# Kernel tuning notes

Measured on AMD Instinct MI355X. Metric: run time of the kernel, lower is better.

## Reference

```python
import jax, jax.numpy as jnp
import numpy as np

N = 50000
E = 640000
D_IN = 128
D_HID = 128
D_S = 64


def setup_inputs() -> dict:
    key = jax.random.key(0)
    ks = jax.random.split(key, 8)
    x = jax.random.normal(ks[0], (N, D_IN), dtype=jnp.float32)
    edge_index = jax.random.randint(ks[1], (2, E), 0, N, dtype=jnp.int64)
    # SAGEConv params: lin_l (applied to aggregated neighbors, has bias), lin_r (root)
    def glorot(k, fan_in, fan_out):
        lim = (6.0 / (fan_in + fan_out)) ** 0.5
        return jax.random.uniform(k, (fan_in, fan_out), jnp.float32, -lim, lim)
    return {
        "x": x,
        "edge_index": edge_index,
        "W_l1": glorot(ks[2], D_IN, D_HID),
        "b_l1": jnp.zeros((D_HID,), jnp.float32),
        "W_r1": glorot(ks[3], D_IN, D_HID),
        "W_l2": glorot(ks[4], D_HID, D_HID),
        "b_l2": jnp.zeros((D_HID,), jnp.float32),
        "W_r2": glorot(ks[5], D_HID, D_HID),
        "W_s": glorot(ks[6], D_HID, D_S),
    }


def _sage_conv(x, src, dst, W_l, b_l, W_r):
    # mean aggregation of source-node features into target nodes
    agg = jax.ops.segment_sum(x[src], dst, num_segments=N)  # [N, d]
    cnt = jax.ops.segment_sum(jnp.ones((src.shape[0],), x.dtype), dst, num_segments=N)
    mean = agg / jnp.maximum(cnt, 1.0)[:, None]
    return mean @ W_l + b_l + x @ W_r


def reference(x, edge_index, W_l1, b_l1, W_r1, W_l2, b_l2, W_r2, W_s):
    src, dst = edge_index[0], edge_index[1]
    h = _sage_conv(x, src, dst, W_l1, b_l1, W_r1)
    h = jax.nn.relu(h)
    h = _sage_conv(h, src, dst, W_l2, b_l2, W_r2)
    out_s = h @ W_s
    return (out_s, h)
```

## Files before the change

### kernel.cpp

```cpp
#include <hip/hip_runtime.h>

#define N_NODES 50000
#define E_EDGES 640000
#define D 128
#define DS 64
#define NTILES 3125
#define BUCKET 64
#define CPAD 16
#define NPART 8
#define PSIZE 6250

typedef __bf16 bf16x8 __attribute__((ext_vector_type(8)));
typedef float f32x4 __attribute__((ext_vector_type(4)));

static __device__ __forceinline__ ushort f2bf(float f) {
    uint u = __float_as_uint(f);
    uint r = u + 0x7fffu + ((u >> 16) & 1u);
    return (ushort)(r >> 16);
}


__global__ void prep_kernel(const float* __restrict__ x,
                            const float* __restrict__ Wl1, const float* __restrict__ Wr1,
                            const float* __restrict__ Wl2, const float* __restrict__ Wr2,
                            const float* __restrict__ Ws,
                            int* __restrict__ cursor, ushort* __restrict__ xb,
                            ushort* __restrict__ WT1f, ushort* __restrict__ WT2f,
                            ushort* __restrict__ WsTf) {
    int tid = blockIdx.x * blockDim.x + threadIdx.x;
    int stride = gridDim.x * blockDim.x;
    for (int i = tid; i < N_NODES * CPAD; i += stride) cursor[i] = 0;
    if (tid < 32768) {
        int n = tid >> 8, k = tid & 255;
        float v = (k < 128) ? Wl1[k * 128 + n] : Wr1[(k - 128) * 128 + n];
        int F = (n >> 4) * 8 + (k >> 5);
        int l = (n & 15) | (((k >> 3) & 3) << 4);
        WT1f[(F * 64 + l) * 8 + (k & 7)] = f2bf(v);
    } else if (tid < 65536) {
        int j = tid - 32768;
        int n = j >> 8, k = j & 255;
        float v = (k < 128) ? Wl2[k * 128 + n] : Wr2[(k - 128) * 128 + n];
        int F = (n >> 4) * 8 + (k >> 5);
        int l = (n & 15) | (((k >> 3) & 3) << 4);
        WT2f[(F * 64 + l) * 8 + (k & 7)] = f2bf(v);
    } else if (tid < 73728) {
        int j = tid - 65536;
        int m = j >> 7, k = j & 127;
        int F = (m >> 4) * 4 + (k >> 5);
        int l = (m & 15) | (((k >> 3) & 3) << 4);
        WsTf[(F * 64 + l) * 8 + (k & 7)] = f2bf(Ws[k * 64 + m]);
    }
    const int n4 = N_NODES * D / 4;
    for (int i = tid; i < n4; i += stride) {
        float4 v = ((const float4*)x)[i];
        ushort4 o;
        o.x = f2bf(v.x); o.y = f2bf(v.y); o.z = f2bf(v.z); o.w = f2bf(v.w);
        ((ushort4*)xb)[i] = o;
    }
}


__global__ void fill_part(const int* __restrict__ src, const int* __restrict__ dst,
                          int* __restrict__ cursor, ushort* __restrict__ esrc, int e) {
    int g = blockIdx.x & (NPART - 1);
    int bchunk = blockIdx.x >> 3;
    int lo = g * PSIZE, hi = lo + PSIZE;
    int nb = gridDim.x >> 3;
    int i = bchunk * blockDim.x + threadIdx.x;
    int stride = nb * blockDim.x;
    for (; i < e; i += stride) {
        int d = dst[i];
        if (d >= lo && d < hi) {
            int pos = atomicAdd(&cursor[d * CPAD], 1);
            if (pos < BUCKET) esrc[d * BUCKET + pos] = (ushort)src[i];
        }
    }
}


__global__ void aggregate_mean_bf16(const ushort* __restrict__ feat, const int* __restrict__ cursor,
                                    const ushort* __restrict__ esrc, ushort* __restrict__ mean, int n) {
    int wid = threadIdx.x >> 6;
    int lane = threadIdx.x & 63;
    int d = blockIdx.x * 4 + wid;
    if (d >= n) return;
    int cnt = cursor[d * CPAD]; if (cnt > BUCKET) cnt = BUCKET;
    int beg = d * BUCKET;
    int g = lane >> 4;
    int gl = lane & 15;

    float acc[8] = {0.f, 0.f, 0.f, 0.f, 0.f, 0.f, 0.f, 0.f};
    for (int i = 0; i < cnt; i += 16) {
        uint4 v[4];
#pragma unroll
        for (int j = 0; j < 4; ++j) {
            int idx = i + g + j * 4;
            v[j] = make_uint4(0u, 0u, 0u, 0u);
            if (idx < cnt) {
                int e = esrc[beg + idx];
                v[j] = ((const uint4*)(feat + (size_t)e * D))[gl];
            }
        }
#pragma unroll
        for (int j = 0; j < 4; ++j) {
            acc[0] += __uint_as_float(v[j].x << 16);
            acc[1] += __uint_as_float(v[j].x & 0xffff0000u);
            acc[2] += __uint_as_float(v[j].y << 16);
            acc[3] += __uint_as_float(v[j].y & 0xffff0000u);
            acc[4] += __uint_as_float(v[j].z << 16);
            acc[5] += __uint_as_float(v[j].z & 0xffff0000u);
            acc[6] += __uint_as_float(v[j].w << 16);
            acc[7] += __uint_as_float(v[j].w & 0xffff0000u);
        }
    }
#pragma unroll
    for (int m = 16; m <= 32; m <<= 1) {
#pragma unroll
        for (int j = 0; j < 8; ++j) acc[j] += __shfl_xor(acc[j], m);
    }
    if (g == 0) {
        float inv = (cnt > 0) ? 1.0f / (float)cnt : 0.0f;
        uint4 o;
        o.x = (uint)f2bf(acc[0] * inv) | ((uint)f2bf(acc[1] * inv) << 16);
        o.y = (uint)f2bf(acc[2] * inv) | ((uint)f2bf(acc[3] * inv) << 16);
        o.z = (uint)f2bf(acc[4] * inv) | ((uint)f2bf(acc[5] * inv) << 16);
        o.w = (uint)f2bf(acc[6] * inv) | ((uint)f2bf(acc[7] * inv) << 16);
        ((uint4*)(mean + (size_t)d * D))[gl] = o;
    }
}


template <bool RELU, bool WF32, bool WBF16, bool OUTS>
__global__ __launch_bounds__(512) void sage_mfma(
    const ushort* __restrict__ A1, const ushort* __restrict__ A2,
    const ushort* __restrict__ WTf, const float* __restrict__ bias,
    float* __restrict__ Hf, ushort* __restrict__ Hb,
    const ushort* __restrict__ WsTf, float* __restrict__ OutS)
{
    __shared__ __attribute__((aligned(16))) char smem[OUTS ? 81920 : 65536];
    int w = threadIdx.x >> 6, lane = threadIdx.x & 63;

#pragma unroll
    for (int it = 0; it < 8; ++it) {
        int off = w * 8192 + it * 1024;
        __builtin_amdgcn_global_load_lds(
            (const __attribute__((address_space(1))) void*)((const char*)WTf + off + lane * 16),
            (__attribute__((address_space(3))) void*)(smem + off), 16, 0, 0);
    }
    if (OUTS) {
#pragma unroll
        for (int it = 0; it < 2; ++it) {
            int off = w * 2048 + it * 1024;
            __builtin_amdgcn_global_load_lds(
                (const __attribute__((address_space(1))) void*)((const char*)WsTf + off + lane * 16),
                (__attribute__((address_space(3))) void*)(smem + 65536 + off), 16, 0, 0);
        }
    }

    int rl = lane & 15;
    int kg = lane >> 4;
    int tile = blockIdx.x * 8 + w;

    bf16x8 a[8];
    if (tile < NTILES) {
        const ushort* r1 = A1 + (size_t)(tile * 16 + rl) * 128 + kg * 8;
        const ushort* r2 = A2 + (size_t)(tile * 16 + rl) * 128 + kg * 8;
#pragma unroll
        for (int s = 0; s < 4; ++s) a[s] = *reinterpret_cast<const bf16x8*>(r1 + s * 32);
#pragma unroll
        for (int s = 0; s < 4; ++s) a[4 + s] = *reinterpret_cast<const bf16x8*>(r2 + s * 32);
    }
    __syncthreads();
    if (tile >= NTILES) return;

    f32x4 acc[8];
#pragma unroll
    for (int f = 0; f < 8; ++f)
        acc[f] = *reinterpret_cast<const f32x4*>(bias + f * 16 + kg * 4);

#pragma unroll
    for (int s = 0; s < 8; ++s) {
#pragma unroll
        for (int f = 0; f < 8; ++f) {
            bf16x8 b = *reinterpret_cast<const bf16x8*>(smem + ((f * 8 + s) * 64 + lane) * 16);
            acc[f] = __builtin_amdgcn_mfma_f32_16x16x32_bf16(b, a[s], acc[f], 0, 0, 0);
        }
    }

    int node = tile * 16 + rl;
#pragma unroll
    for (int f = 0; f < 8; ++f) {
        f32x4 v = acc[f];
        if (RELU) {
            v[0] = fmaxf(v[0], 0.f); v[1] = fmaxf(v[1], 0.f);
            v[2] = fmaxf(v[2], 0.f); v[3] = fmaxf(v[3], 0.f);
        }
        acc[f] = v;
        size_t o = (size_t)node * 128 + f * 16 + kg * 4;
        if (WF32)
            *reinterpret_cast<f32x4*>(Hf + o) = v;
        if (WBF16) {
            ushort4 ob;
            ob.x = f2bf(v[0]); ob.y = f2bf(v[1]); ob.z = f2bf(v[2]); ob.w = f2bf(v[3]);
            *reinterpret_cast<ushort4*>(Hb + o) = ob;
        }
    }

    if (OUTS) {
        uint abx[8], aby[8];
#pragma unroll
        for (int f = 0; f < 8; ++f) {
            abx[f] = (uint)f2bf(acc[f][0]) | ((uint)f2bf(acc[f][1]) << 16);
            aby[f] = (uint)f2bf(acc[f][2]) | ((uint)f2bf(acc[f][3]) << 16);
        }
        int sbase = rl + ((lane & 16) << 1);
        bool top = lane >= 32;
        f32x4 accO[4];
#pragma unroll
        for (int fo = 0; fo < 4; ++fo) accO[fo] = (f32x4){0.f, 0.f, 0.f, 0.f};

#pragma unroll
        for (int s = 0; s < 4; ++s) {
            uint lx = abx[s * 2], ly = aby[s * 2];
            uint hx = abx[s * 2 + 1], hy = aby[s * 2 + 1];
            uint l0 = (uint)__shfl((int)lx, sbase);
            uint h0 = (uint)__shfl((int)hx, sbase);
            uint l1 = (uint)__shfl((int)ly, sbase);
            uint h1 = (uint)__shfl((int)hy, sbase);
            uint l2 = (uint)__shfl((int)lx, sbase + 16);
            uint h2_ = (uint)__shfl((int)hx, sbase + 16);
            uint l3 = (uint)__shfl((int)ly, sbase + 16);
            uint h3 = (uint)__shfl((int)hy, sbase + 16);
            uint q0 = top ? h0 : l0;
            uint q1 = top ? h1 : l1;
            uint q2 = top ? h2_ : l2;
            uint q3 = top ? h3 : l3;
            union { uint4 u; bf16x8 b; } cvt;
            cvt.u = make_uint4(q0, q1, q2, q3);
#pragma unroll
            for (int fo = 0; fo < 4; ++fo) {
                bf16x8 wsA = *reinterpret_cast<const bf16x8*>(
                    smem + 65536 + ((fo * 4 + s) * 64 + lane) * 16);
                accO[fo] = __builtin_amdgcn_mfma_f32_16x16x32_bf16(wsA, cvt.b, accO[fo], 0, 0, 0);
            }
        }
#pragma unroll
        for (int fo = 0; fo < 4; ++fo)
            *reinterpret_cast<f32x4*>(OutS + (size_t)node * DS + fo * 16 + kg * 4) = accO[fo];
    }
}

extern "C" void kernel_launch(void* const* d_in, const int* in_sizes, int n_in,
                              void* d_out, int out_size, void* d_ws, size_t ws_size,
                              hipStream_t stream) {
    const float* x   = (const float*)d_in[0];
    const int*   ei  = (const int*)d_in[1];
    const float* Wl1 = (const float*)d_in[2];
    const float* bl1 = (const float*)d_in[3];
    const float* Wr1 = (const float*)d_in[4];
    const float* Wl2 = (const float*)d_in[5];
    const float* bl2 = (const float*)d_in[6];
    const float* Wr2 = (const float*)d_in[7];
    const float* Ws  = (const float*)d_in[8];

    const int* src = ei;
    const int* dst = ei + E_EDGES;

    char* wsb = (char*)d_ws;
    size_t off = 0;
    auto alloc = [&](size_t bytes) -> void* {
        void* p = wsb + off;
        off = (off + bytes + 255) & ~(size_t)255;
        return p;
    };
    int*    cursor = (int*)alloc(4 * (size_t)N_NODES * CPAD);
    ushort* esrc   = (ushort*)alloc(2 * (size_t)N_NODES * BUCKET);
    ushort* xb     = (ushort*)alloc(2 * (size_t)N_NODES * D);
    ushort* meanb  = (ushort*)alloc(2 * (size_t)N_NODES * D);
    ushort* h1b    = (ushort*)alloc(2 * (size_t)N_NODES * D);
    ushort* WT1f   = (ushort*)alloc(2 * 128 * 256);
    ushort* WT2f   = (ushort*)alloc(2 * 128 * 256);
    ushort* WsTf   = (ushort*)alloc(2 * 64 * 128);

    float* out_s = (float*)d_out;
    float* h2    = (float*)d_out + (size_t)N_NODES * DS;

    prep_kernel<<<2048, 256, 0, stream>>>(x, Wl1, Wr1, Wl2, Wr2, Ws,
                                          cursor, xb, WT1f, WT2f, WsTf);

    fill_part<<<1024, 256, 0, stream>>>(src, dst, cursor, esrc, E_EDGES);

    const int GB = (NTILES + 7) / 8;

    aggregate_mean_bf16<<<(N_NODES + 3) / 4, 256, 0, stream>>>(xb, cursor, esrc, meanb, N_NODES);
    sage_mfma<true, false, true, false><<<GB, 512, 0, stream>>>(
        meanb, xb, WT1f, bl1, nullptr, h1b, nullptr, nullptr);

    aggregate_mean_bf16<<<(N_NODES + 3) / 4, 256, 0, stream>>>(h1b, cursor, esrc, meanb, N_NODES);
    sage_mfma<false, true, false, true><<<GB, 512, 0, stream>>>(
        meanb, h1b, WT2f, bl2, h2, nullptr, WsTf, out_s);
}
```

Baseline: 124.7 us.

## Overlap edge bucketing with bf16 conversion in one combined launch

```diff
diff --git a/kernel.cpp b/kernel.cpp
--- a/kernel.cpp
+++ b/kernel.cpp
@@ -9,9 +9,12 @@
 #define CPAD 16
 #define NPART 8
 #define PSIZE 6250
+#define FILL_BLOCKS 1024
+#define PREP_BLOCKS 1024
 
 typedef __bf16 bf16x8 __attribute__((ext_vector_type(8)));
 typedef float f32x4 __attribute__((ext_vector_type(4)));
+typedef float f32x4v __attribute__((ext_vector_type(4)));
 
 static __device__ __forceinline__ ushort f2bf(float f) {
     uint u = __float_as_uint(f);
@@ -20,59 +23,67 @@
 }
 
 
-__global__ void prep_kernel(const float* __restrict__ x,
-                            const float* __restrict__ Wl1, const float* __restrict__ Wr1,
-                            const float* __restrict__ Wl2, const float* __restrict__ Wr2,
-                            const float* __restrict__ Ws,
-                            int* __restrict__ cursor, ushort* __restrict__ xb,
-                            ushort* __restrict__ WT1f, ushort* __restrict__ WT2f,
-                            ushort* __restrict__ WsTf) {
-    int tid = blockIdx.x * blockDim.x + threadIdx.x;
+__global__ void zero_cursor(int* __restrict__ p, int n) {
+    int i = blockIdx.x * blockDim.x + threadIdx.x;
     int stride = gridDim.x * blockDim.x;
-    for (int i = tid; i < N_NODES * CPAD; i += stride) cursor[i] = 0;
-    if (tid < 32768) {
-        int n = tid >> 8, k = tid & 255;
-        float v = (k < 128) ? Wl1[k * 128 + n] : Wr1[(k - 128) * 128 + n];
-        int F = (n >> 4) * 8 + (k >> 5);
-        int l = (n & 15) | (((k >> 3) & 3) << 4);
-        WT1f[(F * 64 + l) * 8 + (k & 7)] = f2bf(v);
-    } else if (tid < 65536) {
-        int j = tid - 32768;
-        int n = j >> 8, k = j & 255;
-        float v = (k < 128) ? Wl2[k * 128 + n] : Wr2[(k - 128) * 128 + n];
-        int F = (n >> 4) * 8 + (k >> 5);
-        int l = (n & 15) | (((k >> 3) & 3) << 4);
-        WT2f[(F * 64 + l) * 8 + (k & 7)] = f2bf(v);
-    } else if (tid < 73728) {
-        int j = tid - 65536;
-        int m = j >> 7, k = j & 127;
-        int F = (m >> 4) * 4 + (k >> 5);
-        int l = (m & 15) | (((k >> 3) & 3) << 4);
-        WsTf[(F * 64 + l) * 8 + (k & 7)] = f2bf(Ws[k * 64 + m]);
-    }
-    const int n4 = N_NODES * D / 4;
-    for (int i = tid; i < n4; i += stride) {
-        float4 v = ((const float4*)x)[i];
-        ushort4 o;
-        o.x = f2bf(v.x); o.y = f2bf(v.y); o.z = f2bf(v.z); o.w = f2bf(v.w);
-        ((ushort4*)xb)[i] = o;
-    }
-}
-
-
-__global__ void fill_part(const int* __restrict__ src, const int* __restrict__ dst,
-                          int* __restrict__ cursor, ushort* __restrict__ esrc, int e) {
-    int g = blockIdx.x & (NPART - 1);
-    int bchunk = blockIdx.x >> 3;
-    int lo = g * PSIZE, hi = lo + PSIZE;
-    int nb = gridDim.x >> 3;
-    int i = bchunk * blockDim.x + threadIdx.x;
-    int stride = nb * blockDim.x;
-    for (; i < e; i += stride) {
-        int d = dst[i];
-        if (d >= lo && d < hi) {
-            int pos = atomicAdd(&cursor[d * CPAD], 1);
-            if (pos < BUCKET) esrc[d * BUCKET + pos] = (ushort)src[i];
+    for (; i < n; i += stride) p[i] = 0;
+}
+
+
+__global__ void prep_fill(const int* __restrict__ src, const int* __restrict__ dst,
+                          int* __restrict__ cursor, ushort* __restrict__ esrc,
+                          const float* __restrict__ x,
+                          const float* __restrict__ Wl1, const float* __restrict__ Wr1,
+                          const float* __restrict__ Wl2, const float* __restrict__ Wr2,
+                          const float* __restrict__ Ws,
+                          ushort* __restrict__ xb,
+                          ushort* __restrict__ WT1f, ushort* __restrict__ WT2f,
+                          ushort* __restrict__ WsTf) {
+    if (blockIdx.x < FILL_BLOCKS) {
+        int g = blockIdx.x & (NPART - 1);
+        int bchunk = blockIdx.x >> 3;
+        int lo = g * PSIZE, hi = lo + PSIZE;
+        const int nb = FILL_BLOCKS >> 3;
+        int i = bchunk * blockDim.x + threadIdx.x;
+        const int stride = nb * blockDim.x;
+        for (; i < E_EDGES; i += stride) {
+            int d = __builtin_nontemporal_load(dst + i);
+            if (d >= lo && d < hi) {
+                int s = __builtin_nontemporal_load(src + i);
+                int pos = atomicAdd(&cursor[d * CPAD], 1);
+                if (pos < BUCKET) esrc[d * BUCKET + pos] = (ushort)s;
+            }
+        }
+    } else {
+        int bid = blockIdx.x - FILL_BLOCKS;
+        int tid = bid * blockDim.x + threadIdx.x;
+        if (tid < 32768) {
+            int n = tid >> 8, k = tid & 255;
+            float v = (k < 128) ? Wl1[k * 128 + n] : Wr1[(k - 128) * 128 + n];
+            int F = (n >> 4) * 8 + (k >> 5);
+            int l = (n & 15) | (((k >> 3) & 3) << 4);
+            WT1f[(F * 64 + l) * 8 + (k & 7)] = f2bf(v);
+        } else if (tid < 65536) {
+            int j = tid - 32768;
+            int n = j >> 8, k = j & 255;
+            float v = (k < 128) ? Wl2[k * 128 + n] : Wr2[(k - 128) * 128 + n];
+            int F = (n >> 4) * 8 + (k >> 5);
+            int l = (n & 15) | (((k >> 3) & 3) << 4);
+            WT2f[(F * 64 + l) * 8 + (k & 7)] = f2bf(v);
+        } else if (tid < 73728) {
+            int j = tid - 65536;
+            int m = j >> 7, k = j & 127;
+            int F = (m >> 4) * 4 + (k >> 5);
+            int l = (m & 15) | (((k >> 3) & 3) << 4);
+            WsTf[(F * 64 + l) * 8 + (k & 7)] = f2bf(Ws[k * 64 + m]);
+        }
+        const int n4 = N_NODES * D / 4;
+        const int pstride = PREP_BLOCKS * blockDim.x;
+        for (int i = tid; i < n4; i += pstride) {
+            f32x4v v = __builtin_nontemporal_load((const f32x4v*)x + i);
+            ushort4 o;
+            o.x = f2bf(v[0]); o.y = f2bf(v[1]); o.z = f2bf(v[2]); o.w = f2bf(v[3]);
+            ((ushort4*)xb)[i] = o;
         }
     }
 }
@@ -285,10 +296,9 @@
     float* out_s = (float*)d_out;
     float* h2    = (float*)d_out + (size_t)N_NODES * DS;
 
-    prep_kernel<<<2048, 256, 0, stream>>>(x, Wl1, Wr1, Wl2, Wr2, Ws,
-                                          cursor, xb, WT1f, WT2f, WsTf);
-
-    fill_part<<<1024, 256, 0, stream>>>(src, dst, cursor, esrc, E_EDGES);
+    zero_cursor<<<1024, 256, 0, stream>>>(cursor, N_NODES * CPAD);
+    prep_fill<<<FILL_BLOCKS + PREP_BLOCKS, 256, 0, stream>>>(
+        src, dst, cursor, esrc, x, Wl1, Wr1, Wl2, Wr2, Ws, xb, WT1f, WT2f, WsTf);
 
     const int GB = (NTILES + 7) / 8;
 
```

Measured after the change: 140.8 us. 1.13x slower.

## Pre-bin edges by destination partition before scattering into per-node buckets

Applied to the files above, without the earlier changes.

```diff
diff --git a/kernel.cpp b/kernel.cpp
--- a/kernel.cpp
+++ b/kernel.cpp
@@ -9,6 +9,7 @@
 #define CPAD 16
 #define NPART 8
 #define PSIZE 6250
+#define BCAP  98304
 
 typedef __bf16 bf16x8 __attribute__((ext_vector_type(8)));
 typedef float f32x4 __attribute__((ext_vector_type(4)));
@@ -24,12 +25,14 @@
                             const float* __restrict__ Wl1, const float* __restrict__ Wr1,
                             const float* __restrict__ Wl2, const float* __restrict__ Wr2,
                             const float* __restrict__ Ws,
-                            int* __restrict__ cursor, ushort* __restrict__ xb,
+                            int* __restrict__ cursor, int* __restrict__ bincnt,
+                            ushort* __restrict__ xb,
                             ushort* __restrict__ WT1f, ushort* __restrict__ WT2f,
                             ushort* __restrict__ WsTf) {
     int tid = blockIdx.x * blockDim.x + threadIdx.x;
     int stride = gridDim.x * blockDim.x;
     for (int i = tid; i < N_NODES * CPAD; i += stride) cursor[i] = 0;
+    if (tid < NPART * 16) bincnt[tid] = 0;
     if (tid < 32768) {
         int n = tid >> 8, k = tid & 255;
         float v = (k < 128) ? Wl1[k * 128 + n] : Wr1[(k - 128) * 128 + n];
@@ -60,20 +63,49 @@
 }
 
 
-__global__ void fill_part(const int* __restrict__ src, const int* __restrict__ dst,
-                          int* __restrict__ cursor, ushort* __restrict__ esrc, int e) {
+__global__ void bin_pass(const int* __restrict__ src, const int* __restrict__ dst,
+                         int* __restrict__ bincnt, uint* __restrict__ binned, int e) {
+    int lane = threadIdx.x & 63;
+    int i = blockIdx.x * blockDim.x + threadIdx.x;
+    int stride = gridDim.x * blockDim.x;
+    for (; i < e; i += stride) {
+        int d = dst[i];
+        int s = src[i];
+        int myp = d / PSIZE;
+        uint entry = ((uint)d << 16) | (uint)s;
+#pragma unroll
+        for (int p = 0; p < NPART; ++p) {
+            unsigned long long mask = __ballot(myp == p);
+            if (mask) {
+                int leader = __ffsll((long long)mask) - 1;
+                int cnt = __popcll(mask);
+                int base = 0;
+                if (lane == leader) base = atomicAdd(&bincnt[p * 16], cnt);
+                base = __shfl(base, leader);
+                int rank = __popcll(mask & ((1ull << lane) - 1ull));
+                int slot = base + rank;
+                if (myp == p && slot < BCAP) binned[(size_t)p * BCAP + slot] = entry;
+            }
+        }
+    }
+}
+
+
+__global__ void scatter_pass(const uint* __restrict__ binned, const int* __restrict__ bincnt,
+                             int* __restrict__ cursor, ushort* __restrict__ esrc) {
     int g = blockIdx.x & (NPART - 1);
     int bchunk = blockIdx.x >> 3;
-    int lo = g * PSIZE, hi = lo + PSIZE;
     int nb = gridDim.x >> 3;
+    int n = bincnt[g * 16]; if (n > BCAP) n = BCAP;
     int i = bchunk * blockDim.x + threadIdx.x;
     int stride = nb * blockDim.x;
-    for (; i < e; i += stride) {
-        int d = dst[i];
-        if (d >= lo && d < hi) {
-            int pos = atomicAdd(&cursor[d * CPAD], 1);
-            if (pos < BUCKET) esrc[d * BUCKET + pos] = (ushort)src[i];
-        }
+    const uint* bin = binned + (size_t)g * BCAP;
+    for (; i < n; i += stride) {
+        uint e = bin[i];
+        int d = (int)(e >> 16);
+        int s = (int)(e & 0xffffu);
+        int pos = atomicAdd(&cursor[d * CPAD], 1);
+        if (pos < BUCKET) esrc[d * BUCKET + pos] = (ushort)s;
     }
 }
 
@@ -274,6 +306,8 @@
         return p;
     };
     int*    cursor = (int*)alloc(4 * (size_t)N_NODES * CPAD);
+    int*    bincnt = (int*)alloc(4 * (size_t)NPART * 16);
+    uint*   binned = (uint*)alloc(4 * (size_t)NPART * BCAP);
     ushort* esrc   = (ushort*)alloc(2 * (size_t)N_NODES * BUCKET);
     ushort* xb     = (ushort*)alloc(2 * (size_t)N_NODES * D);
     ushort* meanb  = (ushort*)alloc(2 * (size_t)N_NODES * D);
@@ -286,9 +320,10 @@
     float* h2    = (float*)d_out + (size_t)N_NODES * DS;
 
     prep_kernel<<<2048, 256, 0, stream>>>(x, Wl1, Wr1, Wl2, Wr2, Ws,
-                                          cursor, xb, WT1f, WT2f, WsTf);
-
-    fill_part<<<1024, 256, 0, stream>>>(src, dst, cursor, esrc, E_EDGES);
+                                          cursor, bincnt, xb, WT1f, WT2f, WsTf);
+
+    bin_pass<<<1024, 256, 0, stream>>>(src, dst, bincnt, binned, E_EDGES);
+    scatter_pass<<<512, 256, 0, stream>>>(binned, bincnt, cursor, esrc);
 
     const int GB = (NTILES + 7) / 8;
 
```

Result: slower. 438.5 us (+251.6%).

## Split edge bucketing into a shared-memory binning pass and a scatter pass

Applied to the files above, without the earlier changes.

```diff
diff --git a/kernel.cpp b/kernel.cpp
--- a/kernel.cpp
+++ b/kernel.cpp
@@ -9,6 +9,9 @@
 #define CPAD 16
 #define NPART 8
 #define PSIZE 6250
+#define BIN_BLOCKS 256
+#define EPB (E_EDGES / BIN_BLOCKS)
+#define LCAP 512
 
 typedef __bf16 bf16x8 __attribute__((ext_vector_type(8)));
 typedef float f32x4 __attribute__((ext_vector_type(4)));
@@ -60,19 +63,46 @@
 }
 
 
-__global__ void fill_part(const int* __restrict__ src, const int* __restrict__ dst,
-                          int* __restrict__ cursor, ushort* __restrict__ esrc, int e) {
+__global__ __launch_bounds__(256) void bin_pass(const int* __restrict__ src,
+                                                const int* __restrict__ dst,
+                                                int* __restrict__ bincnt,
+                                                uint* __restrict__ binned) {
+    __shared__ uint lbuf[NPART][LCAP];
+    __shared__ int lcnt[NPART];
+    if (threadIdx.x < NPART) lcnt[threadIdx.x] = 0;
+    __syncthreads();
+    int base = blockIdx.x * EPB;
+    for (int i = threadIdx.x; i < EPB; i += blockDim.x) {
+        int d = dst[base + i];
+        int s = src[base + i];
+        int p = d / PSIZE;
+        int pos = atomicAdd(&lcnt[p], 1);
+        if (pos < LCAP) lbuf[p][pos] = ((uint)d << 16) | (uint)s;
+    }
+    __syncthreads();
+    for (int p = 0; p < NPART; ++p) {
+        int n = lcnt[p]; if (n > LCAP) n = LCAP;
+        uint* out = binned + ((size_t)p * BIN_BLOCKS + blockIdx.x) * LCAP;
+        for (int i = threadIdx.x; i < n; i += blockDim.x) out[i] = lbuf[p][i];
+        if (threadIdx.x == 0) bincnt[p * BIN_BLOCKS + blockIdx.x] = n;
+    }
+}
+
+
+__global__ void scatter_pass(const uint* __restrict__ binned, const int* __restrict__ bincnt,
+                             int* __restrict__ cursor, ushort* __restrict__ esrc) {
     int g = blockIdx.x & (NPART - 1);
     int bchunk = blockIdx.x >> 3;
-    int lo = g * PSIZE, hi = lo + PSIZE;
     int nb = gridDim.x >> 3;
-    int i = bchunk * blockDim.x + threadIdx.x;
-    int stride = nb * blockDim.x;
-    for (; i < e; i += stride) {
-        int d = dst[i];
-        if (d >= lo && d < hi) {
+    for (int b = bchunk; b < BIN_BLOCKS; b += nb) {
+        int n = bincnt[g * BIN_BLOCKS + b];
+        const uint* bin = binned + ((size_t)g * BIN_BLOCKS + b) * LCAP;
+        for (int i = threadIdx.x; i < n; i += blockDim.x) {
+            uint e = bin[i];
+            int d = (int)(e >> 16);
+            int s = (int)(e & 0xffffu);
             int pos = atomicAdd(&cursor[d * CPAD], 1);
-            if (pos < BUCKET) esrc[d * BUCKET + pos] = (ushort)src[i];
+            if (pos < BUCKET) esrc[d * BUCKET + pos] = (ushort)s;
         }
     }
 }
@@ -274,6 +304,8 @@
         return p;
     };
     int*    cursor = (int*)alloc(4 * (size_t)N_NODES * CPAD);
+    int*    bincnt = (int*)alloc(4 * (size_t)NPART * BIN_BLOCKS);
+    uint*   binned = (uint*)alloc(4 * (size_t)NPART * BIN_BLOCKS * LCAP);
     ushort* esrc   = (ushort*)alloc(2 * (size_t)N_NODES * BUCKET);
     ushort* xb     = (ushort*)alloc(2 * (size_t)N_NODES * D);
     ushort* meanb  = (ushort*)alloc(2 * (size_t)N_NODES * D);
@@ -288,7 +320,8 @@
     prep_kernel<<<2048, 256, 0, stream>>>(x, Wl1, Wr1, Wl2, Wr2, Ws,
                                           cursor, xb, WT1f, WT2f, WsTf);
 
-    fill_part<<<1024, 256, 0, stream>>>(src, dst, cursor, esrc, E_EDGES);
+    bin_pass<<<BIN_BLOCKS, 256, 0, stream>>>(src, dst, bincnt, binned);
+    scatter_pass<<<512, 256, 0, stream>>>(binned, bincnt, cursor, esrc);
 
     const int GB = (NTILES + 7) / 8;
 
```

Measured after the change: 133.4 us. +6.9%, slower.
